# Performance work log

Measured on AMD Instinct MI355X. Metric: run time of the kernel, lower is better.

## Reference

```python
import jax, jax.numpy as jnp
import numpy as np

NUM_NEIGHBORS = 10
BN_EPS = 1e-5


def setup_inputs() -> dict:
    key = jax.random.key(0)
    ks = jax.random.split(key, 6)
    B, N, D = 8, 4096, 64
    x = jax.random.normal(ks[0], (B, N, D), jnp.float32)

    def w(k, shape):
        return jax.random.normal(k, shape, jnp.float32) * 0.05

    return {
        "x": x,
        "gamma": jnp.ones((D,), jnp.float32),
        "beta": jnp.zeros((D,), jnp.float32),
        "W1": w(ks[1], (128, 128)), "b1": jnp.zeros((128,), jnp.float32),
        "W2": w(ks[2], (128, 64)), "b2": jnp.zeros((64,), jnp.float32),
        "W3": w(ks[3], (64, 64)), "b3": jnp.zeros((64,), jnp.float32),
        "Wg": w(ks[4], (128, 64)), "bg": jnp.zeros((64,), jnp.float32),
    }


def reference(x, gamma, beta, W1, b1, W2, b2, W3, b3, Wg, bg):
    B, N, D = x.shape
    K = NUM_NEIGHBORS

    # BatchNorm1d in train mode: normalize over all B*N rows with batch stats
    xf = x.reshape(-1, D)
    mu = jnp.mean(xf, axis=0)
    var = jnp.mean((xf - mu) ** 2, axis=0)  # biased, as torch BN uses
    xn = (((xf - mu) / jnp.sqrt(var + BN_EPS)) * gamma + beta).reshape(B, N, D)

    # KNN in feature space (standard DGCNN gather_neighbours)
    sq = jnp.sum(xn * xn, axis=-1)  # [B,N]
    dist = sq[:, :, None] + sq[:, None, :] - 2.0 * jnp.einsum("bnd,bmd->bnm", xn, xn)
    _, idx = jax.lax.top_k(-dist, K)  # [B,N,K] indices of nearest (incl. self)

    # gather neighbor features: neigh[b,n,k,:] = xn[b, idx[b,n,k], :]
    neigh = jax.vmap(lambda f, i: f[i])(xn, idx)  # [B,N,K,D]

    exp = jnp.broadcast_to(xn[:, :, None, :], (B, N, K, D))
    edge = jnp.concatenate([exp, exp - neigh], axis=-1)  # [B,N,K,2D]

    h = jax.nn.relu(edge @ W1 + b1)
    h = jax.nn.relu(h @ W2 + b2)
    h = jax.nn.relu(h @ W3 + b3)  # [B,N,K,64]

    vert = jnp.max(h, axis=2)  # max over neighbors -> [B,N,64]
    g = jnp.max(vert, axis=1, keepdims=True)  # global max-pool [B,1,64]
    cat = jnp.concatenate([vert, jnp.broadcast_to(g, vert.shape)], axis=-1)  # [B,N,128]
    return jax.nn.relu(cat @ Wg + bg)  # [B,N,64]
```

## Files before the change

### kernel.cpp

```cpp
#include <hip/hip_runtime.h>
#include <hip/hip_fp16.h>
#include <float.h>

#define BB 8
#define NN 4096
#define DD 64
#define KNBR 10
#define ROWS (BB*NN)

typedef _Float16 f16x8 __attribute__((ext_vector_type(8)));
typedef float f32x4 __attribute__((ext_vector_type(4)));

__global__ void k_bn_stats(const float* __restrict__ x, float* __restrict__ stats) {
  __shared__ float ls[2][4][64];
  int d = threadIdx.x & 63;
  int g = threadIdx.x >> 6;
  float s = 0.f, s2 = 0.f;
  for (int r = blockIdx.x * 4 + g; r < ROWS; r += gridDim.x * 4) {
    float val = x[r * 64 + d];
    s += val;
    s2 = fmaf(val, val, s2);
  }
  ls[0][g][d] = s;
  ls[1][g][d] = s2;
  __syncthreads();
  if (g == 0) {
    atomicAdd(&stats[d],      ls[0][0][d] + ls[0][1][d] + ls[0][2][d] + ls[0][3][d]);
    atomicAdd(&stats[64 + d], ls[1][0][d] + ls[1][1][d] + ls[1][2][d] + ls[1][3][d]);
  }
}

__global__ void k_bn_finalize(const float* __restrict__ stats,
                              const float* __restrict__ gamma,
                              const float* __restrict__ beta,
                              float* __restrict__ ss) {
  int d = threadIdx.x;
  const float inv = 1.f / 32768.f;
  float mu  = stats[d] * inv;
  float var = stats[64 + d] * inv - mu * mu;
  float sc  = gamma[d] / sqrtf(var + 1e-5f);
  ss[d]      = sc;
  ss[64 + d] = beta[d] - mu * sc;
}

__global__ void k_normalize(const float* __restrict__ x, const float* __restrict__ ss,
                            float* __restrict__ xn, float* __restrict__ sq,
                            _Float16* __restrict__ xh, _Float16* __restrict__ xl) {
  int row = blockIdx.x * 4 + (threadIdx.x >> 6);
  int d = threadIdx.x & 63;
  int idx = row * 64 + d;
  float val = fmaf(x[idx], ss[d], ss[64 + d]);
  xn[idx] = val;
  _Float16 h = (_Float16)val;
  _Float16 l = (_Float16)(val - (float)h);
  xh[idx] = h;
  xl[idx] = l;
  float p = val * val;
  #pragma unroll
  for (int off = 32; off > 0; off >>= 1) p += __shfl_xor(p, off);
  if (d == 0) sq[row] = p;
}

__global__ __launch_bounds__(256, 3) void k_knn(const _Float16* __restrict__ xh,
                                                const _Float16* __restrict__ xl,
                                                const float* __restrict__ sq,
                                                int* __restrict__ knn) {
  __shared__ float md[64 * 16 * 10];
  __shared__ float thrs[64];
  __shared__ int cnts[64];
  const int tid = threadIdx.x;
  const int w = tid >> 6, lane = tid & 63;
  const int l15 = lane & 15, lg = lane >> 4;
  const int b = blockIdx.x >> 6;
  const int rowbase = (blockIdx.x & 63) << 6;
  const int bN = b * NN;
  const _Float16* __restrict__ xhb = xh + (size_t)bN * 64;
  const _Float16* __restrict__ xlb = xl + (size_t)bN * 64;
  const float* __restrict__ sqb = sq + bN;

  f16x8 Qh[4][2], Ql[4][2];
  #pragma unroll
  for (int nt = 0; nt < 4; ++nt) {
    #pragma unroll
    for (int ks = 0; ks < 2; ++ks) {
      int qrow = rowbase + nt * 16 + l15;
      Qh[nt][ks] = *(const f16x8*)(xhb + qrow * 64 + ks * 32 + lg * 8);
      Ql[nt][ks] = *(const f16x8*)(xlb + qrow * 64 + ks * 32 + lg * 8);
    }
  }

  float bd[4][10];
  #pragma unroll
  for (int nt = 0; nt < 4; ++nt)
    #pragma unroll
    for (int i = 0; i < 10; ++i) bd[nt][i] = FLT_MAX;

  const int mbase0 = w * 1024;

  #pragma unroll 1
  for (int t = 0; t < 32; ++t) {
    const int mb = mbase0 + t * 32;
    f16x8 Mh[2][2], Ml[2][2];
    #pragma unroll
    for (int mt = 0; mt < 2; ++mt) {
      #pragma unroll
      for (int ks = 0; ks < 2; ++ks) {
        int mrow = mb + mt * 16 + l15;
        Mh[mt][ks] = *(const f16x8*)(xhb + mrow * 64 + ks * 32 + lg * 8);
        Ml[mt][ks] = *(const f16x8*)(xlb + mrow * 64 + ks * 32 + lg * 8);
      }
    }
    f32x4 sqv[2];
    sqv[0] = *(const f32x4*)(sqb + mb + lg * 4);
    sqv[1] = *(const f32x4*)(sqb + mb + 16 + lg * 4);
    #pragma unroll
    for (int nt = 0; nt < 4; ++nt) {
      #pragma unroll
      for (int mt = 0; mt < 2; ++mt) {
        f32x4 a = {0.f, 0.f, 0.f, 0.f};
        #pragma unroll
        for (int ks = 0; ks < 2; ++ks) {
          a = __builtin_amdgcn_mfma_f32_16x16x32_f16(Mh[mt][ks], Qh[nt][ks], a, 0, 0, 0);
          a = __builtin_amdgcn_mfma_f32_16x16x32_f16(Mh[mt][ks], Ql[nt][ks], a, 0, 0, 0);
          a = __builtin_amdgcn_mfma_f32_16x16x32_f16(Ml[mt][ks], Qh[nt][ks], a, 0, 0, 0);
        }
        #pragma unroll
        for (int r = 0; r < 4; ++r) {
          float cd = fmaf(-2.f, a[r], sqv[mt][r]);
          if (cd < bd[nt][9]) {
            float prev = bd[nt][0];
            bd[nt][0] = fminf(cd, bd[nt][0]);
            #pragma unroll
            for (int j = 1; j < 10; ++j) {
              float cur = bd[nt][j];
              bd[nt][j] = fminf(cur, fmaxf(prev, cd));
              prev = cur;
            }
          }
        }
      }
    }
  }

  #pragma unroll
  for (int nt = 0; nt < 4; ++nt)
    #pragma unroll
    for (int i = 0; i < 10; ++i)
      md[((nt * 16 + l15) * 16 + (w * 4 + lg)) * 10 + i] = bd[nt][i];
  if (tid < 64) cnts[tid] = 0;
  __syncthreads();
  if (tid < 64) {
    float fd[10];
    #pragma unroll
    for (int i = 0; i < 10; ++i) fd[i] = FLT_MAX;
    for (int li = 0; li < 16; ++li) {
      #pragma unroll 1
      for (int kk = 0; kk < 10; ++kk) {
        float cd = md[(tid * 16 + li) * 10 + kk];
        if (cd < fd[9]) {
          float prev = fd[0];
          fd[0] = fminf(cd, fd[0]);
          #pragma unroll
          for (int j = 1; j < 10; ++j) {
            float cur = fd[j];
            fd[j] = fminf(cur, fmaxf(prev, cd));
            prev = cur;
          }
        } else break;
      }
    }
    thrs[tid] = fd[9];
  }
  __syncthreads();

  float thv[4];
  #pragma unroll
  for (int nt = 0; nt < 4; ++nt) thv[nt] = thrs[nt * 16 + l15];
  int* knnrow = knn + (size_t)(bN + rowbase) * KNBR;

  #pragma unroll 1
  for (int t = 0; t < 32; ++t) {
    const int mb = mbase0 + t * 32;
    f16x8 Mh[2][2], Ml[2][2];
    #pragma unroll
    for (int mt = 0; mt < 2; ++mt) {
      #pragma unroll
      for (int ks = 0; ks < 2; ++ks) {
        int mrow = mb + mt * 16 + l15;
        Mh[mt][ks] = *(const f16x8*)(xhb + mrow * 64 + ks * 32 + lg * 8);
        Ml[mt][ks] = *(const f16x8*)(xlb + mrow * 64 + ks * 32 + lg * 8);
      }
    }
    f32x4 sqv[2];
    sqv[0] = *(const f32x4*)(sqb + mb + lg * 4);
    sqv[1] = *(const f32x4*)(sqb + mb + 16 + lg * 4);
    #pragma unroll
    for (int nt = 0; nt < 4; ++nt) {
      #pragma unroll
      for (int mt = 0; mt < 2; ++mt) {
        f32x4 a = {0.f, 0.f, 0.f, 0.f};
        #pragma unroll
        for (int ks = 0; ks < 2; ++ks) {
          a = __builtin_amdgcn_mfma_f32_16x16x32_f16(Mh[mt][ks], Qh[nt][ks], a, 0, 0, 0);
          a = __builtin_amdgcn_mfma_f32_16x16x32_f16(Mh[mt][ks], Ql[nt][ks], a, 0, 0, 0);
          a = __builtin_amdgcn_mfma_f32_16x16x32_f16(Ml[mt][ks], Qh[nt][ks], a, 0, 0, 0);
        }
        #pragma unroll
        for (int r = 0; r < 4; ++r) {
          float cd = fmaf(-2.f, a[r], sqv[mt][r]);
          if (cd <= thv[nt]) {
            int qi = nt * 16 + l15;
            int slot = atomicAdd(&cnts[qi], 1);
            if (slot < KNBR)
              knnrow[qi * KNBR + slot] = bN + mb + mt * 16 + lg * 4 + r;
          }
        }
      }
    }
  }
}

__global__ void k_uv(const float* __restrict__ xn, const float* __restrict__ W1,
                     const float* __restrict__ b1, float* __restrict__ u,
                     float* __restrict__ v) {
  __shared__ float xs[64 * 64];
  const int tid = threadIdx.x;
  const int o = tid & 127;
  const bool isU = tid < 128;
  const int rowbase = blockIdx.x * 64;

  float wreg[64];
  #pragma unroll
  for (int d = 0; d < 64; ++d) {
    float bw = W1[(64 + d) * 128 + o];
    wreg[d] = isU ? (W1[d * 128 + o] + bw) : bw;
  }
  const float bb = isU ? b1[o] : 0.f;
  float* __restrict__ dst = isU ? u : v;

  {
    const float4* s4 = (const float4*)(xn + rowbase * 64);
    float4* d4 = (float4*)xs;
    #pragma unroll
    for (int i = 0; i < 4; ++i) d4[tid + 256 * i] = s4[tid + 256 * i];
  }
  __syncthreads();

  for (int r = 0; r < 64; ++r) {
    const float4* xr = (const float4*)(xs + r * 64);
    float a0 = bb, a1 = 0.f, a2 = 0.f, a3 = 0.f;
    #pragma unroll
    for (int q = 0; q < 16; ++q) {
      float4 xv = xr[q];
      a0 = fmaf(xv.x, wreg[4 * q + 0], a0);
      a1 = fmaf(xv.y, wreg[4 * q + 1], a1);
      a2 = fmaf(xv.z, wreg[4 * q + 2], a2);
      a3 = fmaf(xv.w, wreg[4 * q + 3], a3);
    }
    dst[(rowbase + r) * 128 + o] = (a0 + a1) + (a2 + a3);
  }
}

__global__ __launch_bounds__(256, 2) void k_edge(const float* __restrict__ uu,
                                                 const float* __restrict__ vv,
                                                 const int* __restrict__ knn,
                                                 const float* __restrict__ W2,
                                                 const float* __restrict__ b2,
                                                 const float* __restrict__ W3,
                                                 const float* __restrict__ b3,
                                                 float* __restrict__ vert) {
  __shared__ __align__(16) _Float16 W3Ts[64 * 72];
  __shared__ __align__(16) _Float16 h2buf[4][16 * 88];
  __shared__ int vmaxs[4][512];
  const int tid = threadIdx.x;
  const int w = tid >> 6, lane = tid & 63;
  const int l15 = lane & 15, lg = lane >> 4;

  for (int i = tid; i < 64 * 64; i += 256) {
    int o3 = i >> 6, k2 = i & 63;
    W3Ts[o3 * 72 + k2] = (_Float16)W3[k2 * 64 + o3];
  }
  f16x8 w2f[4][4];
  #pragma unroll
  for (int ks = 0; ks < 4; ++ks) {
    #pragma unroll
    for (int nt = 0; nt < 4; ++nt) {
      f16x8 t;
      #pragma unroll
      for (int j = 0; j < 8; ++j)
        t[j] = (_Float16)W2[(ks * 32 + lg * 8 + j) * 64 + nt * 16 + l15];
      w2f[ks][nt] = t;
    }
  }
  float bias2[4], bias3[4];
  #pragma unroll
  for (int nt = 0; nt < 4; ++nt) { bias2[nt] = b2[nt * 16 + l15]; bias3[nt] = b3[nt * 16 + l15]; }

  _Float16* h2w = h2buf[w];
  int* vmaxw = vmaxs[w];
  #pragma unroll
  for (int q = 0; q < 8; ++q) vmaxw[lane * 8 + q] = 0;
  __syncthreads();

  const int wgid = blockIdx.x * 4 + w;
  for (int j = 0; j < 4; ++j) {
    const int g = wgid * 4 + j;
    const int n0 = g * 8;
    const int ebase = n0 * KNBR;
    #pragma unroll 1
    for (int mt = 0; mt < 5; ++mt) {
      const int e = mt * 16 + l15;
      const int m = knn[ebase + e];
      const int n = n0 + e / 10;
      const float* Up = uu + (size_t)n * 128 + lg * 8;
      const float* Vp = vv + (size_t)m * 128 + lg * 8;
      f16x8 A[4];
      #pragma unroll
      for (int ks = 0; ks < 4; ++ks) {
        float4 ua = *(const float4*)(Up + ks * 32);
        float4 ub = *(const float4*)(Up + ks * 32 + 4);
        float4 va = *(const float4*)(Vp + ks * 32);
        float4 vb = *(const float4*)(Vp + ks * 32 + 4);
        f16x8 t;
        t[0] = (_Float16)fmaxf(ua.x - va.x, 0.f);
        t[1] = (_Float16)fmaxf(ua.y - va.y, 0.f);
        t[2] = (_Float16)fmaxf(ua.z - va.z, 0.f);
        t[3] = (_Float16)fmaxf(ua.w - va.w, 0.f);
        t[4] = (_Float16)fmaxf(ub.x - vb.x, 0.f);
        t[5] = (_Float16)fmaxf(ub.y - vb.y, 0.f);
        t[6] = (_Float16)fmaxf(ub.z - vb.z, 0.f);
        t[7] = (_Float16)fmaxf(ub.w - vb.w, 0.f);
        A[ks] = t;
      }
      f32x4 acc[4];
      #pragma unroll
      for (int nt = 0; nt < 4; ++nt) { float bbv = bias2[nt]; acc[nt] = (f32x4){bbv, bbv, bbv, bbv}; }
      #pragma unroll
      for (int ks = 0; ks < 4; ++ks) {
        #pragma unroll
        for (int nt = 0; nt < 4; ++nt)
          acc[nt] = __builtin_amdgcn_mfma_f32_16x16x32_f16(A[ks], w2f[ks][nt], acc[nt], 0, 0, 0);
      }
      #pragma unroll
      for (int nt = 0; nt < 4; ++nt) {
        #pragma unroll
        for (int r = 0; r < 4; ++r)
          h2w[(lg * 4 + r) * 88 + nt * 16 + l15] = (_Float16)fmaxf(acc[nt][r], 0.f);
      }
      f16x8 A3[2];
      #pragma unroll
      for (int ks2 = 0; ks2 < 2; ++ks2)
        A3[ks2] = *(const f16x8*)(h2w + l15 * 88 + ks2 * 32 + lg * 8);
      f32x4 c3[4];
      #pragma unroll
      for (int nt = 0; nt < 4; ++nt) { float bbv = bias3[nt]; c3[nt] = (f32x4){bbv, bbv, bbv, bbv}; }
      #pragma unroll
      for (int ks2 = 0; ks2 < 2; ++ks2) {
        #pragma unroll
        for (int nt = 0; nt < 4; ++nt) {
          f16x8 bf = *(const f16x8*)(W3Ts + (nt * 16 + l15) * 72 + ks2 * 32 + lg * 8);
          c3[nt] = __builtin_amdgcn_mfma_f32_16x16x32_f16(A3[ks2], bf, c3[nt], 0, 0, 0);
        }
      }
      #pragma unroll
      for (int nt = 0; nt < 4; ++nt) {
        #pragma unroll
        for (int r = 0; r < 4; ++r) {
          float val = fmaxf(c3[nt][r], 0.f);
          int e2 = mt * 16 + lg * 4 + r;
          int p = e2 / 10;
          atomicMax(&vmaxw[p * 64 + nt * 16 + l15], __float_as_int(val));
        }
      }
    }
    {
      int p2 = lane >> 3, c0 = (lane & 7) * 8;
      const int* vp = &vmaxw[p2 * 64 + c0];
      float4 r0, r1;
      r0.x = __int_as_float(vp[0]); r0.y = __int_as_float(vp[1]);
      r0.z = __int_as_float(vp[2]); r0.w = __int_as_float(vp[3]);
      r1.x = __int_as_float(vp[4]); r1.y = __int_as_float(vp[5]);
      r1.z = __int_as_float(vp[6]); r1.w = __int_as_float(vp[7]);
      *(float4*)(vert + (size_t)(n0 + p2) * 64 + c0) = r0;
      *(float4*)(vert + (size_t)(n0 + p2) * 64 + c0 + 4) = r1;
      #pragma unroll
      for (int q = 0; q < 8; ++q) vmaxw[lane * 8 + q] = 0;
    }
  }
}

__global__ void k_gmax(const float* __restrict__ vert, float* __restrict__ g) {
  __shared__ float red[4][64];
  int b = blockIdx.x >> 4, chunk = blockIdx.x & 15;
  int sub = threadIdx.x >> 6, o = threadIdx.x & 63;
  float vm = 0.f;
  for (int j = 0; j < 64; ++j) {
    int r = chunk * 256 + j * 4 + sub;
    vm = fmaxf(vm, vert[(b * NN + r) * 64 + o]);
  }
  red[sub][o] = vm;
  __syncthreads();
  if (sub == 0) {
    float mm = fmaxf(fmaxf(red[0][o], red[1][o]), fmaxf(red[2][o], red[3][o]));
    atomicMax((int*)&g[b * 64 + o], __float_as_int(mm));
  }
}

__global__ void k_gb(const float* __restrict__ g, const float* __restrict__ Wg,
                     const float* __restrict__ bg, float* __restrict__ gb) {
  int t = threadIdx.x;
  int b = t >> 6, o = t & 63;
  float acc = bg[o];
  #pragma unroll
  for (int i = 0; i < 64; ++i)
    acc = fmaf(g[b * 64 + i], Wg[(64 + i) * 64 + o], acc);
  gb[b * 64 + o] = acc;
}

__global__ void k_final(const float* __restrict__ vert, const float* __restrict__ Wg,
                        const float* __restrict__ gb, float* __restrict__ out) {
  __shared__ float Wgs[64 * 64];
  int tid = threadIdx.x, w = tid >> 6, lane = tid & 63;
  for (int i = tid; i < 4096; i += 256) Wgs[i] = Wg[i];
  __syncthreads();
  int gw = blockIdx.x * 4 + w;
  for (int j = 0; j < 4; ++j) {
    int n = gw + 8192 * j;
    int b = n >> 12;
    float vrow = vert[n * 64 + lane];
    float ac0 = gb[b * 64 + lane], ac1 = 0.f, ac2 = 0.f, ac3 = 0.f;
    #pragma unroll
    for (int i = 0; i < 64; i += 4) {
      ac0 = fmaf(__shfl(vrow, i),     Wgs[i * 64 + lane],       ac0);
      ac1 = fmaf(__shfl(vrow, i + 1), Wgs[(i + 1) * 64 + lane], ac1);
      ac2 = fmaf(__shfl(vrow, i + 2), Wgs[(i + 2) * 64 + lane], ac2);
      ac3 = fmaf(__shfl(vrow, i + 3), Wgs[(i + 3) * 64 + lane], ac3);
    }
    out[n * 64 + lane] = fmaxf((ac0 + ac1) + (ac2 + ac3), 0.f);
  }
}

extern "C" void kernel_launch(void* const* d_in, const int* in_sizes, int n_in,
                              void* d_out, int out_size, void* d_ws, size_t ws_size,
                              hipStream_t stream) {
  const float* x     = (const float*)d_in[0];
  const float* gamma = (const float*)d_in[1];
  const float* beta  = (const float*)d_in[2];
  const float* W1    = (const float*)d_in[3];
  const float* b1    = (const float*)d_in[4];
  const float* W2    = (const float*)d_in[5];
  const float* b2    = (const float*)d_in[6];
  const float* W3    = (const float*)d_in[7];
  const float* b3    = (const float*)d_in[8];
  const float* Wg    = (const float*)d_in[9];
  const float* bg    = (const float*)d_in[10];
  float* out = (float*)d_out;

  float* ws    = (float*)d_ws;
  float* stats = ws;
  float* ss    = ws + 128;
  float* xn    = ws + 256;
  float* sq    = xn + 2097152;
  int*   knn   = (int*)(sq + 32768);
  float* u     = (float*)(knn + 327680);
  float* v     = u + 4194304;
  float* vert  = v + 4194304;
  float* g     = vert + 2097152;
  float* gb    = g + 512;
  _Float16* xh = (_Float16*)(gb + 512);
  _Float16* xl = (_Float16*)(gb + 512 + 1048576);

  hipMemsetAsync(stats, 0, 128 * sizeof(float), stream);
  hipMemsetAsync(g, 0, 512 * sizeof(float), stream);

  k_bn_stats<<<256, 256, 0, stream>>>(x, stats);
  k_bn_finalize<<<1, 64, 0, stream>>>(stats, gamma, beta, ss);
  k_normalize<<<8192, 256, 0, stream>>>(x, ss, xn, sq, xh, xl);
  k_knn<<<512, 256, 0, stream>>>(xh, xl, sq, knn);
  k_uv<<<512, 256, 0, stream>>>(xn, W1, b1, u, v);
  k_edge<<<256, 256, 0, stream>>>(u, v, knn, W2, b2, W3, b3, vert);
  k_gmax<<<128, 256, 0, stream>>>(vert, g);
  k_gb<<<1, 512, 0, stream>>>(g, Wg, bg, gb);
  k_final<<<2048, 256, 0, stream>>>(vert, Wg, gb, out);
}
```

Measured before the change: 499.2 us.

## Double KNN block to 8 waves and merge per-lane top-k lists via shuffles

The KNN kernel now runs 512 threads per block, so each of 8 waves scans half as many candidate columns, which raises occupancy and parallelism. Partial top-10 lists from the four lane groups in a wave are merged with cross-lane xor shuffles before the shared-memory stage. This shrinks the shared buffer to a padded 89-float row stride and cuts the serial final merge from 16 to 8 lists per row. In exchange it adds shuffle-plus-insertion work in every wave and tightens the register budget under the new launch bounds, which could cause spills.

```diff
diff --git a/kernel.cpp b/kernel.cpp
--- a/kernel.cpp
+++ b/kernel.cpp
@@ -61,11 +61,11 @@
   if (d == 0) sq[row] = p;
 }
 
-__global__ __launch_bounds__(256, 3) void k_knn(const _Float16* __restrict__ xh,
+__global__ __launch_bounds__(512, 4) void k_knn(const _Float16* __restrict__ xh,
                                                 const _Float16* __restrict__ xl,
                                                 const float* __restrict__ sq,
                                                 int* __restrict__ knn) {
-  __shared__ float md[64 * 16 * 10];
+  __shared__ float md[64 * 89];
   __shared__ float thrs[64];
   __shared__ int cnts[64];
   const int tid = threadIdx.x;
@@ -95,10 +95,10 @@
     #pragma unroll
     for (int i = 0; i < 10; ++i) bd[nt][i] = FLT_MAX;
 
-  const int mbase0 = w * 1024;
+  const int mbase0 = w * 512;
 
   #pragma unroll 1
-  for (int t = 0; t < 32; ++t) {
+  for (int t = 0; t < 16; ++t) {
     const int mb = mbase0 + t * 32;
     f16x8 Mh[2][2], Ml[2][2];
     #pragma unroll
@@ -143,20 +143,47 @@
   }
 
   #pragma unroll
-  for (int nt = 0; nt < 4; ++nt)
-    #pragma unroll
-    for (int i = 0; i < 10; ++i)
-      md[((nt * 16 + l15) * 16 + (w * 4 + lg)) * 10 + i] = bd[nt][i];
+  for (int nt = 0; nt < 4; ++nt) {
+    #pragma unroll
+    for (int step = 0; step < 2; ++step) {
+      const int msk = step ? 32 : 16;
+      float ov[10];
+      #pragma unroll
+      for (int i = 0; i < 10; ++i) ov[i] = __shfl_xor(bd[nt][i], msk);
+      #pragma unroll
+      for (int i = 0; i < 10; ++i) {
+        float cd = ov[i];
+        if (cd < bd[nt][9]) {
+          float prev = bd[nt][0];
+          bd[nt][0] = fminf(cd, bd[nt][0]);
+          #pragma unroll
+          for (int j = 1; j < 10; ++j) {
+            float cur = bd[nt][j];
+            bd[nt][j] = fminf(cur, fmaxf(prev, cd));
+            prev = cur;
+          }
+        }
+      }
+    }
+  }
+  if (lg == 0) {
+    #pragma unroll
+    for (int nt = 0; nt < 4; ++nt)
+      #pragma unroll
+      for (int i = 0; i < 10; ++i)
+        md[(nt * 16 + l15) * 89 + w * 11 + i] = bd[nt][i];
+  }
   if (tid < 64) cnts[tid] = 0;
   __syncthreads();
+
   if (tid < 64) {
     float fd[10];
     #pragma unroll
     for (int i = 0; i < 10; ++i) fd[i] = FLT_MAX;
-    for (int li = 0; li < 16; ++li) {
+    for (int li = 0; li < 8; ++li) {
       #pragma unroll 1
       for (int kk = 0; kk < 10; ++kk) {
-        float cd = md[(tid * 16 + li) * 10 + kk];
+        float cd = md[tid * 89 + li * 11 + kk];
         if (cd < fd[9]) {
           float prev = fd[0];
           fd[0] = fminf(cd, fd[0]);
@@ -179,7 +206,7 @@
   int* knnrow = knn + (size_t)(bN + rowbase) * KNBR;
 
   #pragma unroll 1
-  for (int t = 0; t < 32; ++t) {
+  for (int t = 0; t < 16; ++t) {
     const int mb = mbase0 + t * 32;
     f16x8 Mh[2][2], Ml[2][2];
     #pragma unroll
@@ -476,7 +503,7 @@
   k_bn_stats<<<256, 256, 0, stream>>>(x, stats);
   k_bn_finalize<<<1, 64, 0, stream>>>(stats, gamma, beta, ss);
   k_normalize<<<8192, 256, 0, stream>>>(x, ss, xn, sq, xh, xl);
-  k_knn<<<512, 256, 0, stream>>>(xh, xl, sq, knn);
+  k_knn<<<512, 512, 0, stream>>>(xh, xl, sq, knn);
   k_uv<<<512, 256, 0, stream>>>(xn, W1, b1, u, v);
   k_edge<<<256, 256, 0, stream>>>(u, v, knn, W2, b2, W3, b3, vert);
   k_gmax<<<128, 256, 0, stream>>>(vert, g);
```

Measured after the change: 627.0 us. +25.6%, slower.

## Restructure KNN top-k to one query per lane via LDS distance tiles

Applied to the files above, without the earlier changes.

The KNN kernel now uses 512-thread blocks with 8 waves. Each wave computes 64x32 distance tiles with MFMA, writes them to a padded LDS buffer, and then each lane keeps a single 10-entry sorted list for one query row, instead of four lists per lane. This removes the lane divergence and register pressure of the per-lane multi-list insertion, and halves the per-wave candidate range. It also shrinks the final merge to 8 partial lists. Separately, the edge kernel has each wave process one 8-point group instead of four, with the grid grown fourfold to raise parallelism.

```diff
diff --git a/kernel.cpp b/kernel.cpp
--- a/kernel.cpp
+++ b/kernel.cpp
@@ -61,11 +61,11 @@
   if (d == 0) sq[row] = p;
 }
 
-__global__ __launch_bounds__(256, 3) void k_knn(const _Float16* __restrict__ xh,
+__global__ __launch_bounds__(512, 2) void k_knn(const _Float16* __restrict__ xh,
                                                 const _Float16* __restrict__ xl,
                                                 const float* __restrict__ sq,
                                                 int* __restrict__ knn) {
-  __shared__ float md[64 * 16 * 10];
+  __shared__ __align__(16) float Dws[8][2112];
   __shared__ float thrs[64];
   __shared__ int cnts[64];
   const int tid = threadIdx.x;
@@ -78,85 +78,83 @@
   const _Float16* __restrict__ xlb = xl + (size_t)bN * 64;
   const float* __restrict__ sqb = sq + bN;
 
-  f16x8 Qh[4][2], Ql[4][2];
-  #pragma unroll
-  for (int nt = 0; nt < 4; ++nt) {
+  f16x8 Ah[4][2], Al[4][2];
+  #pragma unroll
+  for (int mt = 0; mt < 4; ++mt) {
     #pragma unroll
     for (int ks = 0; ks < 2; ++ks) {
-      int qrow = rowbase + nt * 16 + l15;
-      Qh[nt][ks] = *(const f16x8*)(xhb + qrow * 64 + ks * 32 + lg * 8);
-      Ql[nt][ks] = *(const f16x8*)(xlb + qrow * 64 + ks * 32 + lg * 8);
-    }
-  }
-
-  float bd[4][10];
-  #pragma unroll
-  for (int nt = 0; nt < 4; ++nt)
-    #pragma unroll
-    for (int i = 0; i < 10; ++i) bd[nt][i] = FLT_MAX;
-
-  const int mbase0 = w * 1024;
+      int r = rowbase + mt * 16 + l15;
+      Ah[mt][ks] = *(const f16x8*)(xhb + r * 64 + ks * 32 + lg * 8);
+      Al[mt][ks] = *(const f16x8*)(xlb + r * 64 + ks * 32 + lg * 8);
+    }
+  }
+
+  float bd[10];
+  #pragma unroll
+  for (int i = 0; i < 10; ++i) bd[i] = FLT_MAX;
+
+  float* Dw = Dws[w];
+  float* Drow = Dw + lane * 33;
+  const int mbase0 = w * 512;
 
   #pragma unroll 1
-  for (int t = 0; t < 32; ++t) {
+  for (int t = 0; t < 16; ++t) {
     const int mb = mbase0 + t * 32;
-    f16x8 Mh[2][2], Ml[2][2];
-    #pragma unroll
-    for (int mt = 0; mt < 2; ++mt) {
+    #pragma unroll
+    for (int s = 0; s < 2; ++s) {
+      const int ms = mb + s * 16;
+      f16x8 Bh[2], Bl[2];
       #pragma unroll
       for (int ks = 0; ks < 2; ++ks) {
-        int mrow = mb + mt * 16 + l15;
-        Mh[mt][ks] = *(const f16x8*)(xhb + mrow * 64 + ks * 32 + lg * 8);
-        Ml[mt][ks] = *(const f16x8*)(xlb + mrow * 64 + ks * 32 + lg * 8);
-      }
-    }
-    f32x4 sqv[2];
-    sqv[0] = *(const f32x4*)(sqb + mb + lg * 4);
-    sqv[1] = *(const f32x4*)(sqb + mb + 16 + lg * 4);
-    #pragma unroll
-    for (int nt = 0; nt < 4; ++nt) {
-      #pragma unroll
-      for (int mt = 0; mt < 2; ++mt) {
+        Bh[ks] = *(const f16x8*)(xhb + (ms + l15) * 64 + ks * 32 + lg * 8);
+        Bl[ks] = *(const f16x8*)(xlb + (ms + l15) * 64 + ks * 32 + lg * 8);
+      }
+      float sqv = sqb[ms + l15];
+      #pragma unroll
+      for (int mt = 0; mt < 4; ++mt) {
         f32x4 a = {0.f, 0.f, 0.f, 0.f};
         #pragma unroll
         for (int ks = 0; ks < 2; ++ks) {
-          a = __builtin_amdgcn_mfma_f32_16x16x32_f16(Mh[mt][ks], Qh[nt][ks], a, 0, 0, 0);
-          a = __builtin_amdgcn_mfma_f32_16x16x32_f16(Mh[mt][ks], Ql[nt][ks], a, 0, 0, 0);
-          a = __builtin_amdgcn_mfma_f32_16x16x32_f16(Ml[mt][ks], Qh[nt][ks], a, 0, 0, 0);
+          a = __builtin_amdgcn_mfma_f32_16x16x32_f16(Ah[mt][ks], Bh[ks], a, 0, 0, 0);
+          a = __builtin_amdgcn_mfma_f32_16x16x32_f16(Ah[mt][ks], Bl[ks], a, 0, 0, 0);
+          a = __builtin_amdgcn_mfma_f32_16x16x32_f16(Al[mt][ks], Bh[ks], a, 0, 0, 0);
         }
+        int rw = mt * 16 + lg * 4;
         #pragma unroll
-        for (int r = 0; r < 4; ++r) {
-          float cd = fmaf(-2.f, a[r], sqv[mt][r]);
-          if (cd < bd[nt][9]) {
-            float prev = bd[nt][0];
-            bd[nt][0] = fminf(cd, bd[nt][0]);
-            #pragma unroll
-            for (int j = 1; j < 10; ++j) {
-              float cur = bd[nt][j];
-              bd[nt][j] = fminf(cur, fmaxf(prev, cd));
-              prev = cur;
-            }
-          }
+        for (int r2 = 0; r2 < 4; ++r2)
+          Dw[(rw + r2) * 33 + s * 16 + l15] = fmaf(-2.f, a[r2], sqv);
+      }
+    }
+    #pragma unroll 4
+    for (int mm = 0; mm < 32; ++mm) {
+      float cd = Drow[mm];
+      if (cd < bd[9]) {
+        float prev = bd[0];
+        bd[0] = fminf(cd, bd[0]);
+        #pragma unroll
+        for (int j = 1; j < 10; ++j) {
+          float cur = bd[j];
+          bd[j] = fminf(cur, fmaxf(prev, cd));
+          prev = cur;
         }
       }
     }
   }
 
-  #pragma unroll
-  for (int nt = 0; nt < 4; ++nt)
-    #pragma unroll
-    for (int i = 0; i < 10; ++i)
-      md[((nt * 16 + l15) * 16 + (w * 4 + lg)) * 10 + i] = bd[nt][i];
+  __syncthreads();
+  float* md = &Dws[0][0];
+  #pragma unroll
+  for (int i = 0; i < 10; ++i) md[(w * 64 + lane) * 10 + i] = bd[i];
   if (tid < 64) cnts[tid] = 0;
   __syncthreads();
   if (tid < 64) {
     float fd[10];
     #pragma unroll
     for (int i = 0; i < 10; ++i) fd[i] = FLT_MAX;
-    for (int li = 0; li < 16; ++li) {
+    for (int li = 0; li < 8; ++li) {
       #pragma unroll 1
       for (int kk = 0; kk < 10; ++kk) {
-        float cd = md[(tid * 16 + li) * 10 + kk];
+        float cd = md[(li * 64 + tid) * 10 + kk];
         if (cd < fd[9]) {
           float prev = fd[0];
           fd[0] = fminf(cd, fd[0]);
@@ -173,46 +171,43 @@
   }
   __syncthreads();
 
-  float thv[4];
-  #pragma unroll
-  for (int nt = 0; nt < 4; ++nt) thv[nt] = thrs[nt * 16 + l15];
+  float thv[4][4];
+  #pragma unroll
+  for (int mt = 0; mt < 4; ++mt)
+    #pragma unroll
+    for (int r2 = 0; r2 < 4; ++r2)
+      thv[mt][r2] = thrs[mt * 16 + lg * 4 + r2];
   int* knnrow = knn + (size_t)(bN + rowbase) * KNBR;
 
   #pragma unroll 1
-  for (int t = 0; t < 32; ++t) {
+  for (int t = 0; t < 16; ++t) {
     const int mb = mbase0 + t * 32;
-    f16x8 Mh[2][2], Ml[2][2];
-    #pragma unroll
-    for (int mt = 0; mt < 2; ++mt) {
+    #pragma unroll
+    for (int s = 0; s < 2; ++s) {
+      const int ms = mb + s * 16;
+      f16x8 Bh[2], Bl[2];
       #pragma unroll
       for (int ks = 0; ks < 2; ++ks) {
-        int mrow = mb + mt * 16 + l15;
-        Mh[mt][ks] = *(const f16x8*)(xhb + mrow * 64 + ks * 32 + lg * 8);
-        Ml[mt][ks] = *(const f16x8*)(xlb + mrow * 64 + ks * 32 + lg * 8);
-      }
-    }
-    f32x4 sqv[2];
-    sqv[0] = *(const f32x4*)(sqb + mb + lg * 4);
-    sqv[1] = *(const f32x4*)(sqb + mb + 16 + lg * 4);
-    #pragma unroll
-    for (int nt = 0; nt < 4; ++nt) {
-      #pragma unroll
-      for (int mt = 0; mt < 2; ++mt) {
+        Bh[ks] = *(const f16x8*)(xhb + (ms + l15) * 64 + ks * 32 + lg * 8);
+        Bl[ks] = *(const f16x8*)(xlb + (ms + l15) * 64 + ks * 32 + lg * 8);
+      }
+      float sqv = sqb[ms + l15];
+      #pragma unroll
+      for (int mt = 0; mt < 4; ++mt) {
         f32x4 a = {0.f, 0.f, 0.f, 0.f};
         #pragma unroll
         for (int ks = 0; ks < 2; ++ks) {
-          a = __builtin_amdgcn_mfma_f32_16x16x32_f16(Mh[mt][ks], Qh[nt][ks], a, 0, 0, 0);
-          a = __builtin_amdgcn_mfma_f32_16x16x32_f16(Mh[mt][ks], Ql[nt][ks], a, 0, 0, 0);
-          a = __builtin_amdgcn_mfma_f32_16x16x32_f16(Ml[mt][ks], Qh[nt][ks], a, 0, 0, 0);
+          a = __builtin_amdgcn_mfma_f32_16x16x32_f16(Ah[mt][ks], Bh[ks], a, 0, 0, 0);
+          a = __builtin_amdgcn_mfma_f32_16x16x32_f16(Ah[mt][ks], Bl[ks], a, 0, 0, 0);
+          a = __builtin_amdgcn_mfma_f32_16x16x32_f16(Al[mt][ks], Bh[ks], a, 0, 0, 0);
         }
         #pragma unroll
-        for (int r = 0; r < 4; ++r) {
-          float cd = fmaf(-2.f, a[r], sqv[mt][r]);
-          if (cd <= thv[nt]) {
-            int qi = nt * 16 + l15;
-            int slot = atomicAdd(&cnts[qi], 1);
-            if (slot < KNBR)
-              knnrow[qi * KNBR + slot] = bN + mb + mt * 16 + lg * 4 + r;
+        for (int r2 = 0; r2 < 4; ++r2) {
+          float cd = fmaf(-2.f, a[r2], sqv);
+          if (cd <= thv[mt][r2]) {
+            int row = mt * 16 + lg * 4 + r2;
+            int slot = atomicAdd(&cnts[row], 1);
+            if (slot < KNBR) knnrow[row * KNBR + slot] = bN + ms + l15;
           }
         }
       }
@@ -302,90 +297,85 @@
   for (int q = 0; q < 8; ++q) vmaxw[lane * 8 + q] = 0;
   __syncthreads();
 
-  const int wgid = blockIdx.x * 4 + w;
-  for (int j = 0; j < 4; ++j) {
-    const int g = wgid * 4 + j;
-    const int n0 = g * 8;
-    const int ebase = n0 * KNBR;
-    #pragma unroll 1
-    for (int mt = 0; mt < 5; ++mt) {
-      const int e = mt * 16 + l15;
-      const int m = knn[ebase + e];
-      const int n = n0 + e / 10;
-      const float* Up = uu + (size_t)n * 128 + lg * 8;
-      const float* Vp = vv + (size_t)m * 128 + lg * 8;
-      f16x8 A[4];
-      #pragma unroll
-      for (int ks = 0; ks < 4; ++ks) {
-        float4 ua = *(const float4*)(Up + ks * 32);
-        float4 ub = *(const float4*)(Up + ks * 32 + 4);
-        float4 va = *(const float4*)(Vp + ks * 32);
-        float4 vb = *(const float4*)(Vp + ks * 32 + 4);
-        f16x8 t;
-        t[0] = (_Float16)fmaxf(ua.x - va.x, 0.f);
-        t[1] = (_Float16)fmaxf(ua.y - va.y, 0.f);
-        t[2] = (_Float16)fmaxf(ua.z - va.z, 0.f);
-        t[3] = (_Float16)fmaxf(ua.w - va.w, 0.f);
-        t[4] = (_Float16)fmaxf(ub.x - vb.x, 0.f);
-        t[5] = (_Float16)fmaxf(ub.y - vb.y, 0.f);
-        t[6] = (_Float16)fmaxf(ub.z - vb.z, 0.f);
-        t[7] = (_Float16)fmaxf(ub.w - vb.w, 0.f);
-        A[ks] = t;
-      }
-      f32x4 acc[4];
-      #pragma unroll
-      for (int nt = 0; nt < 4; ++nt) { float bbv = bias2[nt]; acc[nt] = (f32x4){bbv, bbv, bbv, bbv}; }
-      #pragma unroll
-      for (int ks = 0; ks < 4; ++ks) {
-        #pragma unroll
-        for (int nt = 0; nt < 4; ++nt)
-          acc[nt] = __builtin_amdgcn_mfma_f32_16x16x32_f16(A[ks], w2f[ks][nt], acc[nt], 0, 0, 0);
-      }
+  const int g = blockIdx.x * 4 + w;
+  const int n0 = g * 8;
+  const int ebase = n0 * KNBR;
+  #pragma unroll 1
+  for (int mt = 0; mt < 5; ++mt) {
+    const int e = mt * 16 + l15;
+    const int m = knn[ebase + e];
+    const int n = n0 + e / 10;
+    const float* Up = uu + (size_t)n * 128 + lg * 8;
+    const float* Vp = vv + (size_t)m * 128 + lg * 8;
+    f16x8 A[4];
+    #pragma unroll
+    for (int ks = 0; ks < 4; ++ks) {
+      float4 ua = *(const float4*)(Up + ks * 32);
+      float4 ub = *(const float4*)(Up + ks * 32 + 4);
+      float4 va = *(const float4*)(Vp + ks * 32);
+      float4 vb = *(const float4*)(Vp + ks * 32 + 4);
+      f16x8 t;
+      t[0] = (_Float16)fmaxf(ua.x - va.x, 0.f);
+      t[1] = (_Float16)fmaxf(ua.y - va.y, 0.f);
+      t[2] = (_Float16)fmaxf(ua.z - va.z, 0.f);
+      t[3] = (_Float16)fmaxf(ua.w - va.w, 0.f);
+      t[4] = (_Float16)fmaxf(ub.x - vb.x, 0.f);
+      t[5] = (_Float16)fmaxf(ub.y - vb.y, 0.f);
+      t[6] = (_Float16)fmaxf(ub.z - vb.z, 0.f);
+      t[7] = (_Float16)fmaxf(ub.w - vb.w, 0.f);
+      A[ks] = t;
+    }
+    f32x4 acc[4];
+    #pragma unroll
+    for (int nt = 0; nt < 4; ++nt) { float bbv = bias2[nt]; acc[nt] = (f32x4){bbv, bbv, bbv, bbv}; }
+    #pragma unroll
+    for (int ks = 0; ks < 4; ++ks) {
+      #pragma unroll
+      for (int nt = 0; nt < 4; ++nt)
+        acc[nt] = __builtin_amdgcn_mfma_f32_16x16x32_f16(A[ks], w2f[ks][nt], acc[nt], 0, 0, 0);
+    }
+    #pragma unroll
+    for (int nt = 0; nt < 4; ++nt) {
+      #pragma unroll
+      for (int r = 0; r < 4; ++r)
+        h2w[(lg * 4 + r) * 88 + nt * 16 + l15] = (_Float16)fmaxf(acc[nt][r], 0.f);
+    }
+    f16x8 A3[2];
+    #pragma unroll
+    for (int ks2 = 0; ks2 < 2; ++ks2)
+      A3[ks2] = *(const f16x8*)(h2w + l15 * 88 + ks2 * 32 + lg * 8);
+    f32x4 c3[4];
+    #pragma unroll
+    for (int nt = 0; nt < 4; ++nt) { float bbv = bias3[nt]; c3[nt] = (f32x4){bbv, bbv, bbv, bbv}; }
+    #pragma unroll
+    for (int ks2 = 0; ks2 < 2; ++ks2) {
       #pragma unroll
       for (int nt = 0; nt < 4; ++nt) {
-        #pragma unroll
-        for (int r = 0; r < 4; ++r)
-          h2w[(lg * 4 + r) * 88 + nt * 16 + l15] = (_Float16)fmaxf(acc[nt][r], 0.f);
-      }
-      f16x8 A3[2];
-      #pragma unroll
-      for (int ks2 = 0; ks2 < 2; ++ks2)
-        A3[ks2] = *(const f16x8*)(h2w + l15 * 88 + ks2 * 32 + lg * 8);
-      f32x4 c3[4];
-      #pragma unroll
-      for (int nt = 0; nt < 4; ++nt) { float bbv = bias3[nt]; c3[nt] = (f32x4){bbv, bbv, bbv, bbv}; }
-      #pragma unroll
-      for (int ks2 = 0; ks2 < 2; ++ks2) {
-        #pragma unroll
-        for (int nt = 0; nt < 4; ++nt) {
-          f16x8 bf = *(const f16x8*)(W3Ts + (nt * 16 + l15) * 72 + ks2 * 32 + lg * 8);
-          c3[nt] = __builtin_amdgcn_mfma_f32_16x16x32_f16(A3[ks2], bf, c3[nt], 0, 0, 0);
-        }
-      }
-      #pragma unroll
-      for (int nt = 0; nt < 4; ++nt) {
-        #pragma unroll
-        for (int r = 0; r < 4; ++r) {
-          float val = fmaxf(c3[nt][r], 0.f);
-          int e2 = mt * 16 + lg * 4 + r;
-          int p = e2 / 10;
-          atomicMax(&vmaxw[p * 64 + nt * 16 + l15], __float_as_int(val));
-        }
-      }
-    }
-    {
-      int p2 = lane >> 3, c0 = (lane & 7) * 8;
-      const int* vp = &vmaxw[p2 * 64 + c0];
-      float4 r0, r1;
-      r0.x = __int_as_float(vp[0]); r0.y = __int_as_float(vp[1]);
-      r0.z = __int_as_float(vp[2]); r0.w = __int_as_float(vp[3]);
-      r1.x = __int_as_float(vp[4]); r1.y = __int_as_float(vp[5]);
-      r1.z = __int_as_float(vp[6]); r1.w = __int_as_float(vp[7]);
-      *(float4*)(vert + (size_t)(n0 + p2) * 64 + c0) = r0;
-      *(float4*)(vert + (size_t)(n0 + p2) * 64 + c0 + 4) = r1;
-      #pragma unroll
-      for (int q = 0; q < 8; ++q) vmaxw[lane * 8 + q] = 0;
-    }
+        f16x8 bf = *(const f16x8*)(W3Ts + (nt * 16 + l15) * 72 + ks2 * 32 + lg * 8);
+        c3[nt] = __builtin_amdgcn_mfma_f32_16x16x32_f16(A3[ks2], bf, c3[nt], 0, 0, 0);
+      }
+    }
+    #pragma unroll
+    for (int nt = 0; nt < 4; ++nt) {
+      #pragma unroll
+      for (int r = 0; r < 4; ++r) {
+        float val = fmaxf(c3[nt][r], 0.f);
+        int e2 = mt * 16 + lg * 4 + r;
+        int p = e2 / 10;
+        atomicMax(&vmaxw[p * 64 + nt * 16 + l15], __float_as_int(val));
+      }
+    }
+  }
+  {
+    int p2 = lane >> 3, c0 = (lane & 7) * 8;
+    const int* vp = &vmaxw[p2 * 64 + c0];
+    float4 r0, r1;
+    r0.x = __int_as_float(vp[0]); r0.y = __int_as_float(vp[1]);
+    r0.z = __int_as_float(vp[2]); r0.w = __int_as_float(vp[3]);
+    r1.x = __int_as_float(vp[4]); r1.y = __int_as_float(vp[5]);
+    r1.z = __int_as_float(vp[6]); r1.w = __int_as_float(vp[7]);
+    *(float4*)(vert + (size_t)(n0 + p2) * 64 + c0) = r0;
+    *(float4*)(vert + (size_t)(n0 + p2) * 64 + c0 + 4) = r1;
   }
 }
 
@@ -476,9 +466,9 @@
   k_bn_stats<<<256, 256, 0, stream>>>(x, stats);
   k_bn_finalize<<<1, 64, 0, stream>>>(stats, gamma, beta, ss);
   k_normalize<<<8192, 256, 0, stream>>>(x, ss, xn, sq, xh, xl);
-  k_knn<<<512, 256, 0, stream>>>(xh, xl, sq, knn);
+  k_knn<<<512, 512, 0, stream>>>(xh, xl, sq, knn);
   k_uv<<<512, 256, 0, stream>>>(xn, W1, b1, u, v);
-  k_edge<<<256, 256, 0, stream>>>(u, v, knn, W2, b2, W3, b3, vert);
+  k_edge<<<1024, 256, 0, stream>>>(u, v, knn, W2, b2, W3, b3, vert);
   k_gmax<<<128, 256, 0, stream>>>(vert, g);
   k_gb<<<1, 512, 0, stream>>>(g, Wg, bg, gb);
   k_final<<<2048, 256, 0, stream>>>(vert, Wg, gb, out);
```

Result: slower. 523.1 us (+4.8%).
